# Kernel optimization log

Measured on AMD Instinct MI355X. Metric: run time of the kernel, lower is better.

The kernel has to match this reference:

```python
import jax, jax.numpy as jnp
import numpy as np

EPS = 1e-6
SEARCH_RANGE = 4  # K = 2*R+1 = 9


def setup_inputs() -> dict:
    key = jax.random.key(0)
    k1, k2, k3, k4 = jax.random.split(key, 4)
    B, C, H, W = 4, 128, 128, 240
    E = 64
    F_L = jax.random.normal(k1, (B, C, H, W), dtype=jnp.float32)
    F_R = jax.random.normal(k2, (B, C, H, W), dtype=jnp.float32)
    d0 = jax.random.uniform(k3, (B, 1, H, W), dtype=jnp.float32) * 64.0  # pixel disparity
    phi_w = jax.random.normal(k4, (E, C), dtype=jnp.float32) / np.sqrt(C)  # 1x1 conv weight
    return {"F_L": F_L, "F_R": F_R, "d0": d0, "phi_w": phi_w}


def _embed(x, phi_w):
    # 1x1 conv + channel L2 normalize (cosine embedding)
    y = jnp.einsum('ec,bchw->behw', phi_w, x)
    norm = jnp.sqrt(jnp.sum(y * y, axis=1, keepdims=True)) + EPS
    return y / norm


def reference(F_L, F_R, d0, phi_w):
    R = SEARCH_RANGE
    FL = _embed(F_L, phi_w)  # (B,E,H,W)
    FR = _embed(F_R, phi_w)
    B, E, H, W = FL.shape
    deltas = jnp.arange(-R, R + 1, dtype=FL.dtype)  # (K,)
    xx = jnp.arange(W, dtype=FL.dtype)  # base x grid
    # x' = x - (d0 + delta); align_corners=True grid round-trips to pixel coords exactly,
    # y coordinate is identity, so warp is 1D bilinear along W with border clamp.
    xprime = xx[None, None, None, :] - d0[:, None, 0, :, :] - deltas[None, :, None, None]  # (B,K,H,W)
    x0 = jnp.floor(xprime)
    w = xprime - x0  # bilinear weight
    i0 = jnp.clip(x0.astype(jnp.int32), 0, W - 1)
    i1 = jnp.clip(x0.astype(jnp.int32) + 1, 0, W - 1)
    FR_e = FR[:, None]  # (B,1,E,H,W)
    g0 = jnp.take_along_axis(FR_e, i0[:, :, None, :, :], axis=4)  # (B,K,E,H,W)
    g1 = jnp.take_along_axis(FR_e, i1[:, :, None, :, :], axis=4)
    FR_s = g0 * (1.0 - w)[:, :, None] + g1 * w[:, :, None]
    cost_vol = jnp.einsum('behw,bkehw->bkhw', FL, FR_s)  # (B,K,H,W)
    return cost_vol
```

## Files before the change

### kernel.cpp

```cpp
#include <hip/hip_runtime.h>
#include <hip/hip_bf16.h>

#define NB 4
#define NC 128
#define NH 128
#define NW 240
#define NE 64
#define NK 9
#define PLANE (NH*NW)
#define CHW (NC*PLANE)
#define XS 244

typedef __attribute__((ext_vector_type(8))) short short8;
typedef __attribute__((ext_vector_type(4))) float f32x4;

__device__ __forceinline__ unsigned pk2bf(float x, float y){
  __hip_bfloat162 h = __float22bfloat162_rn(make_float2(x, y));
  return *(unsigned*)&h;
}
__device__ __forceinline__ unsigned short f2bf(float f){
  unsigned u = __float_as_uint(f);
  u += 0x7fffu + ((u>>16)&1u);
  return (unsigned short)(u>>16);
}
__device__ __forceinline__ float bfl(unsigned v){ return __uint_as_float(v<<16); }
__device__ __forceinline__ float bfh(unsigned v){ return __uint_as_float(v & 0xffff0000u); }

__global__ __launch_bounds__(1024, 4)
void corr_kernel(const float* __restrict__ xL,
                 const float* __restrict__ xR,
                 const float* __restrict__ d0g,
                 const float* __restrict__ phig,
                 float* __restrict__ outg)
{
  __shared__ __attribute__((aligned(16))) unsigned short xs[NC*XS];
  __shared__ __attribute__((aligned(16))) unsigned short phis[NE*136];
  __shared__ __attribute__((aligned(16))) unsigned short FLb[NW*64];
  __shared__ __attribute__((aligned(16))) unsigned short FRb[NW*64];

  const int tid  = threadIdx.x;
  const int lane = tid & 63;
  const int wv   = tid >> 6;
  const int b    = blockIdx.x >> 7;
  const int h    = blockIdx.x & 127;
  const size_t base = (size_t)b*CHW + (size_t)h*NW;

  float d0v = 0.f;
  if (tid < NW) d0v = d0g[(b*NH + h)*NW + tid];

  #pragma unroll
  for (int i = 0; i < 2; ++i) {
    int idx = i*1024 + tid;
    int e = idx >> 5, q = idx & 31;
    float4 v = *(const float4*)(phig + e*128 + 4*q);
    uint2 pk; pk.x = pk2bf(v.x, v.y); pk.y = pk2bf(v.z, v.w);
    *(uint2*)&phis[e*136 + 4*q] = pk;
  }

  #pragma unroll
  for (int i = 0; i < 8; ++i) {
    int tau = i*1024 + tid;
    int c = tau >> 6, s = tau & 63;
    if (s < 60) {
      float4 v = *(const float4*)(xL + base + (size_t)c*PLANE + 4*s);
      uint2 pk; pk.x = pk2bf(v.x, v.y); pk.y = pk2bf(v.z, v.w);
      *(uint2*)&xs[c*XS + 4*s] = pk;
    }
  }
  __syncthreads();

  const int mrow = lane & 15;
  const int kg   = lane >> 4;
  const int nt   = wv;

  auto gemm_norm = [&](unsigned short* dst) {
    f32x4 acc[4];
    #pragma unroll
    for (int mt = 0; mt < 4; ++mt) acc[mt] = (f32x4){0.f,0.f,0.f,0.f};

    if (nt < 15) {
      const int col = 16*nt + mrow;
      #pragma unroll
      for (int ks = 0; ks < 4; ++ks) {
        const int r0 = 32*ks + 8*kg;
        short8 bfv;
        #pragma unroll
        for (int j = 0; j < 8; ++j)
          bfv[j] = (short)xs[(r0 + j)*XS + col];
        #pragma unroll
        for (int mt = 0; mt < 4; ++mt) {
          short8 af = *(const short8*)&phis[(16*mt + mrow)*136 + 32*ks + 8*kg];
          acc[mt] = __builtin_amdgcn_mfma_f32_16x16x32_bf16(af, bfv, acc[mt], 0, 0, 0);
        }
      }
      float ss = 0.f;
      #pragma unroll
      for (int mt = 0; mt < 4; ++mt)
        #pragma unroll
        for (int r = 0; r < 4; ++r)
          ss += acc[mt][r]*acc[mt][r];
      ss += __shfl_xor(ss, 16, 64);
      ss += __shfl_xor(ss, 32, 64);
      float inv = 1.f/(sqrtf(ss) + 1e-6f);
      int n = 16*nt + mrow;
      #pragma unroll
      for (int mt = 0; mt < 4; ++mt) {
        int e0 = 16*mt + 4*kg;
        ushort4 pk;
        pk.x = f2bf(acc[mt][0]*inv);
        pk.y = f2bf(acc[mt][1]*inv);
        pk.z = f2bf(acc[mt][2]*inv);
        pk.w = f2bf(acc[mt][3]*inv);
        int pos = n*64 + (((e0>>3) ^ (n&7))<<3) + (e0&7);
        *(ushort4*)&dst[pos] = pk;
      }
    }
  };

  gemm_norm(FLb);
  __syncthreads();

  #pragma unroll
  for (int i = 0; i < 8; ++i) {
    int tau = i*1024 + tid;
    int c = tau >> 6, s = tau & 63;
    if (s < 60) {
      float4 v = *(const float4*)(xR + base + (size_t)c*PLANE + 4*s);
      uint2 pk; pk.x = pk2bf(v.x, v.y); pk.y = pk2bf(v.z, v.w);
      *(uint2*)&xs[c*XS + 4*s] = pk;
    }
  }
  __syncthreads();

  gemm_norm(FRb);
  __syncthreads();

  if (tid < NW) {
    const int p = tid;
    float xf  = (float)p - d0v;
    float x0  = floorf(xf);
    float wfr = xf - x0;
    int jb = (int)x0 - 4;

    float fl[64];
    #pragma unroll
    for (int c = 0; c < 8; ++c) {
      uint4 raw = *(const uint4*)&FLb[p*64 + ((c ^ (p&7))<<3)];
      fl[8*c+0]=bfl(raw.x); fl[8*c+1]=bfh(raw.x);
      fl[8*c+2]=bfl(raw.y); fl[8*c+3]=bfh(raw.y);
      fl[8*c+4]=bfl(raw.z); fl[8*c+5]=bfh(raw.z);
      fl[8*c+6]=bfl(raw.w); fl[8*c+7]=bfh(raw.w);
    }

    float D[10];
    #pragma unroll
    for (int t = 0; t < 10; ++t) {
      int j = jb + t;
      j = j < 0 ? 0 : (j > NW-1 ? NW-1 : j);
      float s = 0.f;
      #pragma unroll
      for (int c = 0; c < 8; ++c) {
        uint4 raw = *(const uint4*)&FRb[j*64 + ((c ^ (j&7))<<3)];
        s += fl[8*c+0]*bfl(raw.x) + fl[8*c+1]*bfh(raw.x)
           + fl[8*c+2]*bfl(raw.y) + fl[8*c+3]*bfh(raw.y)
           + fl[8*c+4]*bfl(raw.z) + fl[8*c+5]*bfh(raw.z)
           + fl[8*c+6]*bfl(raw.w) + fl[8*c+7]*bfh(raw.w);
      }
      D[t] = s;
    }

    size_t ob = (size_t)(b*NK)*PLANE + (size_t)h*NW + p;
    #pragma unroll
    for (int k = 0; k < NK; ++k) {
      int t0 = 8 - k;
      float cv = (1.f - wfr)*D[t0] + wfr*D[t0+1];
      outg[ob + (size_t)k*PLANE] = cv;
    }
  }
}

extern "C" void kernel_launch(void* const* d_in, const int* in_sizes, int n_in,
                              void* d_out, int out_size, void* d_ws, size_t ws_size,
                              hipStream_t stream) {
  const float* xL   = (const float*)d_in[0];
  const float* xR   = (const float*)d_in[1];
  const float* d0g  = (const float*)d_in[2];
  const float* phig = (const float*)d_in[3];
  float* outg = (float*)d_out;
  corr_kernel<<<dim3(NB*NH), dim3(1024), 0, stream>>>(xL, xR, d0g, phig, outg);
}
```

Before: 158.0 us.

## Split fused kernel into separate embed and cost-volume kernels via workspace

Replaces the single fused kernel with two launches. The first embeds left and right rows independently, giving twice as many smaller blocks with more concurrent loads. Its bf16 embeddings go to a workspace buffer, which a second lightweight kernel reads back to compute the cost volume. The aim is more parallelism and overlap of the large input reads. The cost is an extra launch plus a write and re-read of about 16 MB of intermediate data, and the fused kernel remains as a fallback when the workspace is too small.

```diff
diff --git a/kernel.cpp b/kernel.cpp
--- a/kernel.cpp
+++ b/kernel.cpp
@@ -10,6 +10,7 @@
 #define PLANE (NH*NW)
 #define CHW (NC*PLANE)
 #define XS 244
+#define EMB_ELEMS (NB*NH*NW*NE)
 
 typedef __attribute__((ext_vector_type(8))) short short8;
 typedef __attribute__((ext_vector_type(4))) float f32x4;
@@ -26,12 +27,178 @@
 __device__ __forceinline__ float bfl(unsigned v){ return __uint_as_float(v<<16); }
 __device__ __forceinline__ float bfh(unsigned v){ return __uint_as_float(v & 0xffff0000u); }
 
+__global__ __launch_bounds__(512, 4)
+void embed_kernel(const float* __restrict__ xL,
+                  const float* __restrict__ xR,
+                  const float* __restrict__ phig,
+                  unsigned short* __restrict__ emb)
+{
+  __shared__ __attribute__((aligned(16))) unsigned short xs[NC*XS];
+  __shared__ __attribute__((aligned(16))) unsigned short phis[NE*136];
+
+  const int tid  = threadIdx.x;
+  const int lane = tid & 63;
+  const int wv   = tid >> 6;
+  const int t    = blockIdx.x >> 9;
+  const int bh   = blockIdx.x & 511;
+  const float* __restrict__ src = t ? xR : xL;
+  const size_t base = (size_t)(bh >> 7)*CHW + (size_t)(bh & 127)*NW;
+  unsigned short* __restrict__ outp = emb + (size_t)t*EMB_ELEMS + (size_t)bh*(NW*NE);
+
+  #pragma unroll
+  for (int i = 0; i < 4; ++i) {
+    int idx = i*512 + tid;
+    int e = idx >> 5, q = idx & 31;
+    float4 v = *(const float4*)(phig + e*128 + 4*q);
+    uint2 pk; pk.x = pk2bf(v.x, v.y); pk.y = pk2bf(v.z, v.w);
+    *(uint2*)&phis[e*136 + 4*q] = pk;
+  }
+  #pragma unroll
+  for (int i = 0; i < 15; ++i) {
+    int idx = i*512 + tid;
+    int c = idx / 60, s = idx - 60*c;
+    float4 v = *(const float4*)(src + base + (size_t)c*PLANE + 4*s);
+    uint2 pk; pk.x = pk2bf(v.x, v.y); pk.y = pk2bf(v.z, v.w);
+    *(uint2*)&xs[c*XS + 4*s] = pk;
+  }
+  __syncthreads();
+
+  const int mrow = lane & 15;
+  const int kg   = lane >> 4;
+
+  #pragma unroll
+  for (int it = 0; it < 2; ++it) {
+    const int nt = wv*2 + it;
+    if (nt >= 15) continue;
+    f32x4 acc[4];
+    #pragma unroll
+    for (int mt = 0; mt < 4; ++mt) acc[mt] = (f32x4){0.f,0.f,0.f,0.f};
+    const int col = 16*nt + mrow;
+    #pragma unroll
+    for (int ks = 0; ks < 4; ++ks) {
+      const int r0 = 32*ks + 8*kg;
+      short8 bfv;
+      #pragma unroll
+      for (int j = 0; j < 8; ++j)
+        bfv[j] = (short)xs[(r0 + j)*XS + col];
+      #pragma unroll
+      for (int mt = 0; mt < 4; ++mt) {
+        short8 af = *(const short8*)&phis[(16*mt + mrow)*136 + 32*ks + 8*kg];
+        acc[mt] = __builtin_amdgcn_mfma_f32_16x16x32_bf16(af, bfv, acc[mt], 0, 0, 0);
+      }
+    }
+    float ss = 0.f;
+    #pragma unroll
+    for (int mt = 0; mt < 4; ++mt)
+      #pragma unroll
+      for (int r = 0; r < 4; ++r)
+        ss += acc[mt][r]*acc[mt][r];
+    ss += __shfl_xor(ss, 16, 64);
+    ss += __shfl_xor(ss, 32, 64);
+    float inv = 1.f/(sqrtf(ss) + 1e-6f);
+    const int n = 16*nt + mrow;
+    #pragma unroll
+    for (int mt = 0; mt < 4; ++mt) {
+      int e0 = 16*mt + 4*kg;
+      ushort4 pk;
+      pk.x = f2bf(acc[mt][0]*inv);
+      pk.y = f2bf(acc[mt][1]*inv);
+      pk.z = f2bf(acc[mt][2]*inv);
+      pk.w = f2bf(acc[mt][3]*inv);
+      *(ushort4*)&outp[n*NE + e0] = pk;
+    }
+  }
+}
+
+__global__ __launch_bounds__(256, 4)
+void cost_kernel(const unsigned short* __restrict__ emb,
+                 const float* __restrict__ d0g,
+                 float* __restrict__ outg)
+{
+  __shared__ __attribute__((aligned(16))) unsigned short FLb[NW*64];
+  __shared__ __attribute__((aligned(16))) unsigned short FRb[NW*64];
+
+  const int tid = threadIdx.x;
+  const int bh  = blockIdx.x;
+  const int b   = bh >> 7;
+  const int h   = bh & 127;
+
+  float d0v = 0.f;
+  if (tid < NW) d0v = d0g[bh*NW + tid];
+
+  const unsigned short* __restrict__ FLg = emb + (size_t)bh*(NW*NE);
+  const unsigned short* __restrict__ FRg = emb + (size_t)EMB_ELEMS + (size_t)bh*(NW*NE);
+
+  #pragma unroll
+  for (int i = 0; i < 8; ++i) {
+    int idx = i*256 + tid;
+    if (idx < 1920) {
+      uint4 v = *(const uint4*)(FLg + idx*8);
+      int p = idx >> 3, c = idx & 7;
+      *(uint4*)&FLb[p*64 + ((c ^ (p&7))<<3)] = v;
+    }
+  }
+  #pragma unroll
+  for (int i = 0; i < 8; ++i) {
+    int idx = i*256 + tid;
+    if (idx < 1920) {
+      uint4 v = *(const uint4*)(FRg + idx*8);
+      int p = idx >> 3, c = idx & 7;
+      *(uint4*)&FRb[p*64 + ((c ^ (p&7))<<3)] = v;
+    }
+  }
+  __syncthreads();
+
+  if (tid < NW) {
+    const int p = tid;
+    float xf  = (float)p - d0v;
+    float x0  = floorf(xf);
+    float wfr = xf - x0;
+    int jb = (int)x0 - 4;
+
+    float fl[64];
+    #pragma unroll
+    for (int c = 0; c < 8; ++c) {
+      uint4 raw = *(const uint4*)&FLb[p*64 + ((c ^ (p&7))<<3)];
+      fl[8*c+0]=bfl(raw.x); fl[8*c+1]=bfh(raw.x);
+      fl[8*c+2]=bfl(raw.y); fl[8*c+3]=bfh(raw.y);
+      fl[8*c+4]=bfl(raw.z); fl[8*c+5]=bfh(raw.z);
+      fl[8*c+6]=bfl(raw.w); fl[8*c+7]=bfh(raw.w);
+    }
+
+    float D[10];
+    #pragma unroll
+    for (int t = 0; t < 10; ++t) {
+      int j = jb + t;
+      j = j < 0 ? 0 : (j > NW-1 ? NW-1 : j);
+      float s = 0.f;
+      #pragma unroll
+      for (int c = 0; c < 8; ++c) {
+        uint4 raw = *(const uint4*)&FRb[j*64 + ((c ^ (j&7))<<3)];
+        s += fl[8*c+0]*bfl(raw.x) + fl[8*c+1]*bfh(raw.x)
+           + fl[8*c+2]*bfl(raw.y) + fl[8*c+3]*bfh(raw.y)
+           + fl[8*c+4]*bfl(raw.z) + fl[8*c+5]*bfh(raw.z)
+           + fl[8*c+6]*bfl(raw.w) + fl[8*c+7]*bfh(raw.w);
+      }
+      D[t] = s;
+    }
+
+    size_t ob = (size_t)(b*NK)*PLANE + (size_t)h*NW + p;
+    #pragma unroll
+    for (int k = 0; k < NK; ++k) {
+      int t0 = 8 - k;
+      float cv = (1.f - wfr)*D[t0] + wfr*D[t0+1];
+      outg[ob + (size_t)k*PLANE] = cv;
+    }
+  }
+}
+
 __global__ __launch_bounds__(1024, 4)
-void corr_kernel(const float* __restrict__ xL,
-                 const float* __restrict__ xR,
-                 const float* __restrict__ d0g,
-                 const float* __restrict__ phig,
-                 float* __restrict__ outg)
+void corr_fused(const float* __restrict__ xL,
+                const float* __restrict__ xR,
+                const float* __restrict__ d0g,
+                const float* __restrict__ phig,
+                float* __restrict__ outg)
 {
   __shared__ __attribute__((aligned(16))) unsigned short xs[NC*XS];
   __shared__ __attribute__((aligned(16))) unsigned short phis[NE*136];
@@ -56,7 +223,6 @@
     uint2 pk; pk.x = pk2bf(v.x, v.y); pk.y = pk2bf(v.z, v.w);
     *(uint2*)&phis[e*136 + 4*q] = pk;
   }
-
   #pragma unroll
   for (int i = 0; i < 8; ++i) {
     int tau = i*1024 + tid;
@@ -77,7 +243,6 @@
     f32x4 acc[4];
     #pragma unroll
     for (int mt = 0; mt < 4; ++mt) acc[mt] = (f32x4){0.f,0.f,0.f,0.f};
-
     if (nt < 15) {
       const int col = 16*nt + mrow;
       #pragma unroll
@@ -119,7 +284,6 @@
 
   gemm_norm(FLb);
   __syncthreads();
-
   #pragma unroll
   for (int i = 0; i < 8; ++i) {
     int tau = i*1024 + tid;
@@ -131,7 +295,6 @@
     }
   }
   __syncthreads();
-
   gemm_norm(FRb);
   __syncthreads();
 
@@ -141,7 +304,6 @@
     float x0  = floorf(xf);
     float wfr = xf - x0;
     int jb = (int)x0 - 4;
-
     float fl[64];
     #pragma unroll
     for (int c = 0; c < 8; ++c) {
@@ -151,7 +313,6 @@
       fl[8*c+4]=bfl(raw.z); fl[8*c+5]=bfh(raw.z);
       fl[8*c+6]=bfl(raw.w); fl[8*c+7]=bfh(raw.w);
     }
-
     float D[10];
     #pragma unroll
     for (int t = 0; t < 10; ++t) {
@@ -168,7 +329,6 @@
       }
       D[t] = s;
     }
-
     size_t ob = (size_t)(b*NK)*PLANE + (size_t)h*NW + p;
     #pragma unroll
     for (int k = 0; k < NK; ++k) {
@@ -187,5 +347,13 @@
   const float* d0g  = (const float*)d_in[2];
   const float* phig = (const float*)d_in[3];
   float* outg = (float*)d_out;
-  corr_kernel<<<dim3(NB*NH), dim3(1024), 0, stream>>>(xL, xR, d0g, phig, outg);
-}
+
+  const size_t need = (size_t)2 * EMB_ELEMS * sizeof(unsigned short);
+  if (ws_size >= need) {
+    unsigned short* emb = (unsigned short*)d_ws;
+    embed_kernel<<<dim3(2*NB*NH), dim3(512), 0, stream>>>(xL, xR, phig, emb);
+    cost_kernel<<<dim3(NB*NH), dim3(256), 0, stream>>>(emb, d0g, outg);
+  } else {
+    corr_fused<<<dim3(NB*NH), dim3(1024), 0, stream>>>(xL, xR, d0g, phig, outg);
+  }
+}
```

Result: slower. 161.7 us (+2.4%).

## Split into embed and cost kernels with double-buffered channel-chunk loads

Applied to the files above, without the earlier changes.

The fused per-row kernel is split into two kernels. An embed kernel, launched with twice as many blocks (one per image row per side), computes the normalized bf16 embeddings and writes them to workspace. It loads input channels in 32-channel chunks and double-buffers them in LDS, so the global loads for the next chunk overlap the MFMA work on the current one. Each wave now handles two column tiles, and the smaller LDS footprint allows more resident blocks. A separate cost kernel reads the embeddings back into swizzled LDS and computes the cost volume, which adds a global round-trip of the embeddings and a second launch.

```diff
diff --git a/kernel.cpp b/kernel.cpp
--- a/kernel.cpp
+++ b/kernel.cpp
@@ -10,6 +10,8 @@
 #define PLANE (NH*NW)
 #define CHW (NC*PLANE)
 #define XS 244
+#define KC 32
+#define EMB_ELEMS (NB*NH*NW*NE)
 
 typedef __attribute__((ext_vector_type(8))) short short8;
 typedef __attribute__((ext_vector_type(4))) float f32x4;
@@ -26,113 +28,169 @@
 __device__ __forceinline__ float bfl(unsigned v){ return __uint_as_float(v<<16); }
 __device__ __forceinline__ float bfh(unsigned v){ return __uint_as_float(v & 0xffff0000u); }
 
-__global__ __launch_bounds__(1024, 4)
-void corr_kernel(const float* __restrict__ xL,
-                 const float* __restrict__ xR,
-                 const float* __restrict__ d0g,
-                 const float* __restrict__ phig,
-                 float* __restrict__ outg)
+__global__ __launch_bounds__(512, 6)
+void embed_kernel(const float* __restrict__ xL,
+                  const float* __restrict__ xR,
+                  const float* __restrict__ phig,
+                  unsigned short* __restrict__ emb)
 {
-  __shared__ __attribute__((aligned(16))) unsigned short xs[NC*XS];
+  __shared__ __attribute__((aligned(16))) unsigned short xs[2][KC*XS];
   __shared__ __attribute__((aligned(16))) unsigned short phis[NE*136];
-  __shared__ __attribute__((aligned(16))) unsigned short FLb[NW*64];
-  __shared__ __attribute__((aligned(16))) unsigned short FRb[NW*64];
 
   const int tid  = threadIdx.x;
   const int lane = tid & 63;
   const int wv   = tid >> 6;
-  const int b    = blockIdx.x >> 7;
-  const int h    = blockIdx.x & 127;
-  const size_t base = (size_t)b*CHW + (size_t)h*NW;
-
-  float d0v = 0.f;
-  if (tid < NW) d0v = d0g[(b*NH + h)*NW + tid];
-
-  #pragma unroll
-  for (int i = 0; i < 2; ++i) {
-    int idx = i*1024 + tid;
+  const int t    = blockIdx.x >> 9;
+  const int bh   = blockIdx.x & 511;
+  const float* __restrict__ src = t ? xR : xL;
+  const size_t base = (size_t)(bh >> 7)*CHW + (size_t)(bh & 127)*NW;
+  unsigned short* __restrict__ outp = emb + (size_t)t*EMB_ELEMS + (size_t)bh*(NW*NE);
+
+  auto issue_chunk = [&](int ch, float4* r){
+    #pragma unroll
+    for (int i = 0; i < 4; ++i) {
+      int idx = i*512 + tid;
+      int c = idx >> 6, s = idx & 63;
+      if (s < 60)
+        r[i] = *(const float4*)(src + base + (size_t)(ch*KC + c)*PLANE + 4*s);
+    }
+  };
+  auto write_chunk = [&](int buf, const float4* r){
+    #pragma unroll
+    for (int i = 0; i < 4; ++i) {
+      int idx = i*512 + tid;
+      int c = idx >> 6, s = idx & 63;
+      if (s < 60) {
+        uint2 pk; pk.x = pk2bf(r[i].x, r[i].y); pk.y = pk2bf(r[i].z, r[i].w);
+        *(uint2*)&xs[buf][c*XS + 4*s] = pk;
+      }
+    }
+  };
+
+  float4 creg[4];
+  issue_chunk(0, creg);
+  float4 ph[4];
+  #pragma unroll
+  for (int i = 0; i < 4; ++i) {
+    int idx = i*512 + tid;
     int e = idx >> 5, q = idx & 31;
-    float4 v = *(const float4*)(phig + e*128 + 4*q);
-    uint2 pk; pk.x = pk2bf(v.x, v.y); pk.y = pk2bf(v.z, v.w);
+    ph[i] = *(const float4*)(phig + e*128 + 4*q);
+  }
+  write_chunk(0, creg);
+  #pragma unroll
+  for (int i = 0; i < 4; ++i) {
+    int idx = i*512 + tid;
+    int e = idx >> 5, q = idx & 31;
+    uint2 pk; pk.x = pk2bf(ph[i].x, ph[i].y); pk.y = pk2bf(ph[i].z, ph[i].w);
     *(uint2*)&phis[e*136 + 4*q] = pk;
-  }
-
-  #pragma unroll
-  for (int i = 0; i < 8; ++i) {
-    int tau = i*1024 + tid;
-    int c = tau >> 6, s = tau & 63;
-    if (s < 60) {
-      float4 v = *(const float4*)(xL + base + (size_t)c*PLANE + 4*s);
-      uint2 pk; pk.x = pk2bf(v.x, v.y); pk.y = pk2bf(v.z, v.w);
-      *(uint2*)&xs[c*XS + 4*s] = pk;
-    }
   }
   __syncthreads();
 
   const int mrow = lane & 15;
   const int kg   = lane >> 4;
-  const int nt   = wv;
-
-  auto gemm_norm = [&](unsigned short* dst) {
-    f32x4 acc[4];
-    #pragma unroll
-    for (int mt = 0; mt < 4; ++mt) acc[mt] = (f32x4){0.f,0.f,0.f,0.f};
-
-    if (nt < 15) {
-      const int col = 16*nt + mrow;
-      #pragma unroll
-      for (int ks = 0; ks < 4; ++ks) {
-        const int r0 = 32*ks + 8*kg;
+  const int nt0  = wv*2;
+
+  f32x4 acc[2][4];
+  #pragma unroll
+  for (int it = 0; it < 2; ++it)
+    #pragma unroll
+    for (int mt = 0; mt < 4; ++mt)
+      acc[it][mt] = (f32x4){0.f,0.f,0.f,0.f};
+
+  #pragma unroll
+  for (int ch = 0; ch < 4; ++ch) {
+    if (ch < 3) issue_chunk(ch+1, creg);
+
+    short8 af[4];
+    #pragma unroll
+    for (int mt = 0; mt < 4; ++mt)
+      af[mt] = *(const short8*)&phis[(16*mt + mrow)*136 + 32*ch + 8*kg];
+
+    #pragma unroll
+    for (int it = 0; it < 2; ++it) {
+      const int nt = nt0 + it;
+      if (nt < 15) {
+        const int col = 16*nt + mrow;
         short8 bfv;
         #pragma unroll
         for (int j = 0; j < 8; ++j)
-          bfv[j] = (short)xs[(r0 + j)*XS + col];
+          bfv[j] = (short)xs[ch & 1][(8*kg + j)*XS + col];
         #pragma unroll
-        for (int mt = 0; mt < 4; ++mt) {
-          short8 af = *(const short8*)&phis[(16*mt + mrow)*136 + 32*ks + 8*kg];
-          acc[mt] = __builtin_amdgcn_mfma_f32_16x16x32_bf16(af, bfv, acc[mt], 0, 0, 0);
-        }
+        for (int mt = 0; mt < 4; ++mt)
+          acc[it][mt] = __builtin_amdgcn_mfma_f32_16x16x32_bf16(af[mt], bfv, acc[it][mt], 0, 0, 0);
       }
-      float ss = 0.f;
+    }
+
+    if (ch < 3) {
+      write_chunk((ch+1) & 1, creg);
+      __syncthreads();
+    }
+  }
+
+  #pragma unroll
+  for (int it = 0; it < 2; ++it) {
+    const int nt = nt0 + it;
+    if (nt >= 15) continue;
+    float ss = 0.f;
+    #pragma unroll
+    for (int mt = 0; mt < 4; ++mt)
       #pragma unroll
-      for (int mt = 0; mt < 4; ++mt)
-        #pragma unroll
-        for (int r = 0; r < 4; ++r)
-          ss += acc[mt][r]*acc[mt][r];
-      ss += __shfl_xor(ss, 16, 64);
-      ss += __shfl_xor(ss, 32, 64);
-      float inv = 1.f/(sqrtf(ss) + 1e-6f);
-      int n = 16*nt + mrow;
-      #pragma unroll
-      for (int mt = 0; mt < 4; ++mt) {
-        int e0 = 16*mt + 4*kg;
-        ushort4 pk;
-        pk.x = f2bf(acc[mt][0]*inv);
-        pk.y = f2bf(acc[mt][1]*inv);
-        pk.z = f2bf(acc[mt][2]*inv);
-        pk.w = f2bf(acc[mt][3]*inv);
-        int pos = n*64 + (((e0>>3) ^ (n&7))<<3) + (e0&7);
-        *(ushort4*)&dst[pos] = pk;
-      }
-    }
-  };
-
-  gemm_norm(FLb);
-  __syncthreads();
+      for (int r = 0; r < 4; ++r)
+        ss += acc[it][mt][r]*acc[it][mt][r];
+    ss += __shfl_xor(ss, 16, 64);
+    ss += __shfl_xor(ss, 32, 64);
+    float inv = 1.f/(sqrtf(ss) + 1e-6f);
+    const int n = 16*nt + mrow;
+    #pragma unroll
+    for (int mt = 0; mt < 4; ++mt) {
+      int e0 = 16*mt + 4*kg;
+      ushort4 pk;
+      pk.x = f2bf(acc[it][mt][0]*inv);
+      pk.y = f2bf(acc[it][mt][1]*inv);
+      pk.z = f2bf(acc[it][mt][2]*inv);
+      pk.w = f2bf(acc[it][mt][3]*inv);
+      *(ushort4*)&outp[n*NE + e0] = pk;
+    }
+  }
+}
+
+__global__ __launch_bounds__(256, 4)
+void cost_kernel(const unsigned short* __restrict__ emb,
+                 const float* __restrict__ d0g,
+                 float* __restrict__ outg)
+{
+  __shared__ __attribute__((aligned(16))) unsigned short FLb[NW*64];
+  __shared__ __attribute__((aligned(16))) unsigned short FRb[NW*64];
+
+  const int tid = threadIdx.x;
+  const int bh  = blockIdx.x;
+  const int b   = bh >> 7;
+  const int h   = bh & 127;
+
+  float d0v = 0.f;
+  if (tid < NW) d0v = d0g[bh*NW + tid];
+
+  const unsigned short* __restrict__ FLg = emb + (size_t)bh*(NW*NE);
+  const unsigned short* __restrict__ FRg = emb + (size_t)EMB_ELEMS + (size_t)bh*(NW*NE);
 
   #pragma unroll
   for (int i = 0; i < 8; ++i) {
-    int tau = i*1024 + tid;
-    int c = tau >> 6, s = tau & 63;
-    if (s < 60) {
-      float4 v = *(const float4*)(xR + base + (size_t)c*PLANE + 4*s);
-      uint2 pk; pk.x = pk2bf(v.x, v.y); pk.y = pk2bf(v.z, v.w);
-      *(uint2*)&xs[c*XS + 4*s] = pk;
-    }
-  }
-  __syncthreads();
-
-  gemm_norm(FRb);
+    int idx = i*256 + tid;
+    if (idx < 1920) {
+      uint4 v = *(const uint4*)(FLg + idx*8);
+      int p = idx >> 3, c = idx & 7;
+      *(uint4*)&FLb[p*64 + ((c ^ (p&7))<<3)] = v;
+    }
+  }
+  #pragma unroll
+  for (int i = 0; i < 8; ++i) {
+    int idx = i*256 + tid;
+    if (idx < 1920) {
+      uint4 v = *(const uint4*)(FRg + idx*8);
+      int p = idx >> 3, c = idx & 7;
+      *(uint4*)&FRb[p*64 + ((c ^ (p&7))<<3)] = v;
+    }
+  }
   __syncthreads();
 
   if (tid < NW) {
@@ -187,5 +245,8 @@
   const float* d0g  = (const float*)d_in[2];
   const float* phig = (const float*)d_in[3];
   float* outg = (float*)d_out;
-  corr_kernel<<<dim3(NB*NH), dim3(1024), 0, stream>>>(xL, xR, d0g, phig, outg);
-}
+
+  unsigned short* embp = (unsigned short*)d_ws;
+  embed_kernel<<<dim3(2*NB*NH), dim3(512), 0, stream>>>(xL, xR, phig, embp);
+  cost_kernel<<<dim3(NB*NH), dim3(256), 0, stream>>>(embp, d0g, outg);
+}
```

Result: slower. 281.3 us (+78.1%).
